# Performance work log

Hardware: AMD Instinct MI355X
Metric: run time of the kernel (lower is better)

The kernel has to match this reference:

```python
import jax, jax.numpy as jnp
import numpy as np

EPS = 1e-05
ITERS = 3


def safe_norm(s, axis):
    return jnp.sqrt(jnp.sum(s * s, axis=axis, keepdims=True) + EPS)


def squash(s, axis):
    norm = safe_norm(s, axis)
    return (norm / (1.0 + norm)) * s / norm


def setup_inputs() -> dict:
    key = jax.random.key(0)
    k1, k2 = jax.random.split(key)
    b, B, C, P, h, w = 4, 288, 32, 16, 14, 14  # B = K*K*32, P = pose 4x4
    u = jax.random.normal(k1, (b, B, C, P, h, w), dtype=jnp.float32)
    a = jax.random.uniform(k2, (b, B, h, w), dtype=jnp.float32)
    return {"u": u, "a": a}


def reference(u, a):
    # mode='dynamic': activation a is unused by this routing variant.
    # max_min_norm over pose axis (3), max/min over input-capsule axis (1)
    norm = safe_norm(u, 3)                          # (b,B,C,1,h,w)
    max_n = jnp.max(norm, axis=1, keepdims=True)    # (b,1,C,1,h,w)
    min_n = jnp.min(norm, axis=1, keepdims=True)
    u = u / (max_n - min_n)

    b, B, C, P, h, w = u.shape
    r = jnp.zeros((b, B, C, 1, h, w), dtype=u.dtype)
    v = None
    for i in range(ITERS):
        c = jax.nn.softmax(r, axis=2)                               # over C
        v = squash(jnp.sum(c * u, axis=1, keepdims=True), 3)        # (b,1,C,P,h,w)
        if i != ITERS - 1:
            r = r + jnp.sum(u * v, axis=3, keepdims=True)           # agreement
    a_out = safe_norm(v, 3)                                         # (b,1,C,1,h,w)
    return (jnp.squeeze(v, 1), jnp.squeeze(jnp.squeeze(a_out, 1), 2))
```

## Files before the change

### kernel.cpp

```cpp
#include <hip/hip_runtime.h>


constexpr int kB    = 4;
constexpr int kIC   = 288;
constexpr int kOC   = 32;
constexpr int kP    = 16;
constexpr int kHW   = 196;
constexpr int kNPOS = kB * kHW;
constexpr int kTILE = 16;
constexpr int kNTILES = kNPOS / kTILE;
constexpr int kNCH  = 16;
constexpr int kBCH  = kIC / kNCH;
constexpr int kSCP  = kOC * kP * kNPOS;
constexpr int kSC   = kOC * kNPOS;
constexpr int kBStride = kOC * kP * kHW;
constexpr float kEPS = 1e-5f;

__global__ __launch_bounds__(512, 4) void pass1_kernel(
    const float* __restrict__ U, float* __restrict__ s0,
    unsigned int* __restrict__ maxb, unsigned int* __restrict__ minb)
{
    const int tid = threadIdx.x;
    const int pos = tid & (kTILE - 1);
    const int c   = tid >> 4;
    const int n   = blockIdx.x * kTILE + pos;
    const int b   = n / kHW;
    const int hw  = n - b * kHW;
    const int B0  = blockIdx.y * kBCH;
    const float* up = U + (size_t)(((b * kIC + B0) * kOC + c) * kP) * kHW + hw;

    float sacc[kP];
#pragma unroll
    for (int p = 0; p < kP; ++p) sacc[p] = 0.f;
    float mx = 0.f, mn = 3.4e38f;

    for (int Bi = 0; Bi < kBCH; ++Bi) {
        float u[kP];
#pragma unroll
        for (int p = 0; p < kP; ++p) u[p] = up[p * kHW];
        float nsq = kEPS;
#pragma unroll
        for (int p = 0; p < kP; ++p) { nsq = fmaf(u[p], u[p], nsq); sacc[p] += u[p]; }
        const float nr = sqrtf(nsq);
        mx = fmaxf(mx, nr);
        mn = fminf(mn, nr);
        up += kBStride;
    }
    const int cn = c * kNPOS + n;
    atomicMax(&maxb[cn], __float_as_uint(mx));
    atomicMin(&minb[cn], __float_as_uint(mn));
#pragma unroll
    for (int p = 0; p < kP; ++p)
        atomicAdd(&s0[(c * kP + p) * kNPOS + n], sacc[p]);
}

__global__ void v0_kernel(float* __restrict__ s0,
                          const unsigned int* __restrict__ maxb,
                          const unsigned int* __restrict__ minb,
                          float* __restrict__ scaleb)
{
    const int i = blockIdx.x * blockDim.x + threadIdx.x;
    if (i >= kSC) return;
    const int c = i / kNPOS;
    const int n = i - c * kNPOS;
    const float mx = __uint_as_float(maxb[i]);
    const float mn = __uint_as_float(minb[i]);
    const float sc = 1.f / (mx - mn);
    scaleb[i] = sc;
    float sv[kP];
    float nsq = kEPS;
#pragma unroll
    for (int p = 0; p < kP; ++p) {
        const float v = s0[(c * kP + p) * kNPOS + n] * sc * (1.f / 32.f);
        sv[p] = v;
        nsq = fmaf(v, v, nsq);
    }
    const float inv = 1.f / (1.f + sqrtf(nsq));
#pragma unroll
    for (int p = 0; p < kP; ++p)
        s0[(c * kP + p) * kNPOS + n] = sv[p] * inv;
}

__global__ __launch_bounds__(512, 4) void route_kernel(
    const float* __restrict__ U, const float* __restrict__ Vr,
    const float* __restrict__ scaleb, float* __restrict__ sout)
{
    __shared__ float ldsM[8 * kTILE];
    __shared__ float ldsS[8 * kTILE];
    const int tid = threadIdx.x;
    const int pos = tid & (kTILE - 1);
    const int c   = tid >> 4;
    const int wv  = tid >> 6;
    const int n   = blockIdx.x * kTILE + pos;
    const int b   = n / kHW;
    const int hw  = n - b * kHW;
    const int B0  = blockIdx.y * kBCH;
    const float* up = U + (size_t)(((b * kIC + B0) * kOC + c) * kP) * kHW + hw;

    float vr[kP];
#pragma unroll
    for (int p = 0; p < kP; ++p) vr[p] = Vr[(c * kP + p) * kNPOS + n];
    const float sc = scaleb[c * kNPOS + n];

    float acc[kP];
#pragma unroll
    for (int p = 0; p < kP; ++p) acc[p] = 0.f;

    for (int Bi = 0; Bi < kBCH; ++Bi) {
        float u[kP];
#pragma unroll
        for (int p = 0; p < kP; ++p) u[p] = up[p * kHW];
        float d = 0.f;
#pragma unroll
        for (int p = 0; p < kP; ++p) d = fmaf(u[p], vr[p], d);
        const float r = sc * d;

        float m = r;
        m = fmaxf(m, __shfl_xor(m, 16));
        m = fmaxf(m, __shfl_xor(m, 32));
        if ((tid & 63) < kTILE) ldsM[wv * kTILE + pos] = m;
        __syncthreads();
        float mxv = ldsM[pos];
#pragma unroll
        for (int w = 1; w < 8; ++w) mxv = fmaxf(mxv, ldsM[w * kTILE + pos]);

        const float e = __expf(r - mxv);
        float z = e;
        z += __shfl_xor(z, 16);
        z += __shfl_xor(z, 32);
        if ((tid & 63) < kTILE) ldsS[wv * kTILE + pos] = z;
        __syncthreads();
        float Z = ldsS[pos];
#pragma unroll
        for (int w = 1; w < 8; ++w) Z += ldsS[w * kTILE + pos];

        const float cb = e / Z;
#pragma unroll
        for (int p = 0; p < kP; ++p) acc[p] = fmaf(cb, u[p], acc[p]);
        up += kBStride;
    }
#pragma unroll
    for (int p = 0; p < kP; ++p)
        atomicAdd(&sout[(c * kP + p) * kNPOS + n], sc * acc[p]);
}

__global__ void v1_kernel(float* __restrict__ v0buf,
                          const float* __restrict__ s1)
{
    const int i = blockIdx.x * blockDim.x + threadIdx.x;
    if (i >= kSC) return;
    const int c = i / kNPOS;
    const int n = i - c * kNPOS;
    float sv[kP];
    float nsq = kEPS;
#pragma unroll
    for (int p = 0; p < kP; ++p) {
        const float v = s1[(c * kP + p) * kNPOS + n];
        sv[p] = v;
        nsq = fmaf(v, v, nsq);
    }
    const float inv = 1.f / (1.f + sqrtf(nsq));
#pragma unroll
    for (int p = 0; p < kP; ++p)
        v0buf[(c * kP + p) * kNPOS + n] += sv[p] * inv;
}

__global__ void final_kernel(const float* __restrict__ s2, float* __restrict__ out)
{
    const int i = blockIdx.x * blockDim.x + threadIdx.x;
    if (i >= kSC) return;
    const int c = i / kNPOS;
    const int n = i - c * kNPOS;
    const int b = n / kHW;
    const int hw = n - b * kHW;
    float sv[kP];
    float nsq = kEPS;
#pragma unroll
    for (int p = 0; p < kP; ++p) {
        const float v = s2[(c * kP + p) * kNPOS + n];
        sv[p] = v;
        nsq = fmaf(v, v, nsq);
    }
    const float inv = 1.f / (1.f + sqrtf(nsq));
    float vs = 0.f;
#pragma unroll
    for (int p = 0; p < kP; ++p) {
        const float v = sv[p] * inv;
        out[(size_t)((b * kOC + c) * kP + p) * kHW + hw] = v;
        vs = fmaf(v, v, vs);
    }
    out[(size_t)kSCP + (b * kOC + c) * kHW + hw] = sqrtf(vs + kEPS);
}

extern "C" void kernel_launch(void* const* d_in, const int* in_sizes, int n_in,
                              void* d_out, int out_size, void* d_ws, size_t ws_size,
                              hipStream_t stream) {
    const float* U = (const float*)d_in[0];
    float* out = (float*)d_out;
    float* ws  = (float*)d_ws;

    float* s0 = ws;
    float* s1 = ws + kSCP;
    float* s2 = ws + 2 * kSCP;
    unsigned int* maxb = (unsigned int*)(ws + 3 * kSCP);
    unsigned int* minb = maxb + kSC;
    float* scaleb = (float*)(minb + kSC);

    hipMemsetAsync(s0, 0, (size_t)3 * kSCP * sizeof(float), stream);
    hipMemsetAsync(maxb, 0, (size_t)kSC * sizeof(unsigned int), stream);
    hipMemsetAsync(minb, 0x7F, (size_t)kSC * sizeof(unsigned int), stream);

    dim3 grid(kNTILES, kNCH);
    pass1_kernel<<<grid, 512, 0, stream>>>(U, s0, maxb, minb);
    v0_kernel<<<(kSC + 255) / 256, 256, 0, stream>>>(s0, maxb, minb, scaleb);
    route_kernel<<<grid, 512, 0, stream>>>(U, s0, scaleb, s1);
    v1_kernel<<<(kSC + 255) / 256, 256, 0, stream>>>(s0, s1);
    route_kernel<<<grid, 512, 0, stream>>>(U, s0, scaleb, s2);
    final_kernel<<<(kSC + 255) / 256, 256, 0, stream>>>(s2, out);
}
```

Baseline: 1.068 ms.

## Process two positions per thread with float2 loads and remap block order

Each thread now handles a pair of adjacent spatial positions and loads them as float2, widening the global loads of U in both pass1 and route kernels. The grid becomes 1D, and blocks are remapped through a stride-8 permutation, likely to spread tiles and chunks across XCDs or L2 slices. Route launch bounds are relaxed from 4 to 3 blocks per SM to allow more registers for the doubled state. The trade is higher register pressure and fewer blocks (400 vs 784), which lowers parallelism and adds a tail tile with clamped, masked positions.

```diff
diff --git a/kernel.cpp b/kernel.cpp
--- a/kernel.cpp
+++ b/kernel.cpp
@@ -7,51 +7,74 @@
 constexpr int kP    = 16;
 constexpr int kHW   = 196;
 constexpr int kNPOS = kB * kHW;
-constexpr int kTILE = 16;
-constexpr int kNTILES = kNPOS / kTILE;
+constexpr int kPAIR = 16;
+constexpr int kNTILES = 25;
 constexpr int kNCH  = 16;
 constexpr int kBCH  = kIC / kNCH;
 constexpr int kSCP  = kOC * kP * kNPOS;
 constexpr int kSC   = kOC * kNPOS;
-constexpr int kBStride = kOC * kP * kHW;
+constexpr int kBStride2 = kOC * kP * kHW / 2;
+constexpr int kNBLK = kNTILES * kNCH;
 constexpr float kEPS = 1e-5f;
+
+__device__ inline void decomp(int l, int& tile, int& chunk) {
+    const int logical = (l & 7) * (kNBLK / 8) + (l >> 3);
+    tile  = logical >> 4;
+    chunk = logical & 15;
+}
 
 __global__ __launch_bounds__(512, 4) void pass1_kernel(
     const float* __restrict__ U, float* __restrict__ s0,
     unsigned int* __restrict__ maxb, unsigned int* __restrict__ minb)
 {
+    int tile, chunk;
+    decomp(blockIdx.x, tile, chunk);
     const int tid = threadIdx.x;
-    const int pos = tid & (kTILE - 1);
+    const int j   = tid & 15;
     const int c   = tid >> 4;
-    const int n   = blockIdx.x * kTILE + pos;
-    const int b   = n / kHW;
-    const int hw  = n - b * kHW;
-    const int B0  = blockIdx.y * kBCH;
-    const float* up = U + (size_t)(((b * kIC + B0) * kOC + c) * kP) * kHW + hw;
-
-    float sacc[kP];
-#pragma unroll
-    for (int p = 0; p < kP; ++p) sacc[p] = 0.f;
-    float mx = 0.f, mn = 3.4e38f;
+    int n0 = tile * 32 + 2 * j;
+    const bool valid = (n0 < kNPOS);
+    if (!valid) n0 = kNPOS - 2;
+    const int b  = n0 / kHW;
+    const int hw = n0 - b * kHW;
+    const int B0 = chunk * kBCH;
+    const float2* up = (const float2*)(U + (size_t)(((b * kIC + B0) * kOC + c) * kP) * kHW + hw);
+
+    float2 sacc[kP];
+#pragma unroll
+    for (int p = 0; p < kP; ++p) sacc[p] = make_float2(0.f, 0.f);
+    float2 mx = make_float2(0.f, 0.f);
+    float2 mn = make_float2(3.4e38f, 3.4e38f);
 
     for (int Bi = 0; Bi < kBCH; ++Bi) {
-        float u[kP];
-#pragma unroll
-        for (int p = 0; p < kP; ++p) u[p] = up[p * kHW];
-        float nsq = kEPS;
-#pragma unroll
-        for (int p = 0; p < kP; ++p) { nsq = fmaf(u[p], u[p], nsq); sacc[p] += u[p]; }
-        const float nr = sqrtf(nsq);
-        mx = fmaxf(mx, nr);
-        mn = fminf(mn, nr);
-        up += kBStride;
-    }
-    const int cn = c * kNPOS + n;
-    atomicMax(&maxb[cn], __float_as_uint(mx));
-    atomicMin(&minb[cn], __float_as_uint(mn));
-#pragma unroll
-    for (int p = 0; p < kP; ++p)
-        atomicAdd(&s0[(c * kP + p) * kNPOS + n], sacc[p]);
+        float2 u[kP];
+#pragma unroll
+        for (int p = 0; p < kP; ++p) u[p] = up[p * (kHW / 2)];
+        float2 nsq = make_float2(kEPS, kEPS);
+#pragma unroll
+        for (int p = 0; p < kP; ++p) {
+            nsq.x = fmaf(u[p].x, u[p].x, nsq.x);
+            nsq.y = fmaf(u[p].y, u[p].y, nsq.y);
+            sacc[p].x += u[p].x;
+            sacc[p].y += u[p].y;
+        }
+        const float nrx = sqrtf(nsq.x), nry = sqrtf(nsq.y);
+        mx.x = fmaxf(mx.x, nrx); mx.y = fmaxf(mx.y, nry);
+        mn.x = fminf(mn.x, nrx); mn.y = fminf(mn.y, nry);
+        up += kBStride2;
+    }
+    if (valid) {
+        const int cn = c * kNPOS + n0;
+        atomicMax(&maxb[cn],     __float_as_uint(mx.x));
+        atomicMax(&maxb[cn + 1], __float_as_uint(mx.y));
+        atomicMin(&minb[cn],     __float_as_uint(mn.x));
+        atomicMin(&minb[cn + 1], __float_as_uint(mn.y));
+#pragma unroll
+        for (int p = 0; p < kP; ++p) {
+            atomicAdd(&s0[(c * kP + p) * kNPOS + n0],     sacc[p].x);
+            atomicAdd(&s0[(c * kP + p) * kNPOS + n0 + 1], sacc[p].y);
+        }
+    }
 }
 
 __global__ void v0_kernel(float* __restrict__ s0,
@@ -81,67 +104,86 @@
         s0[(c * kP + p) * kNPOS + n] = sv[p] * inv;
 }
 
-__global__ __launch_bounds__(512, 4) void route_kernel(
+__global__ __launch_bounds__(512, 3) void route_kernel(
     const float* __restrict__ U, const float* __restrict__ Vr,
     const float* __restrict__ scaleb, float* __restrict__ sout)
 {
-    __shared__ float ldsM[8 * kTILE];
-    __shared__ float ldsS[8 * kTILE];
+    __shared__ float2 ldsM[8 * kPAIR];
+    __shared__ float2 ldsS[8 * kPAIR];
+    int tile, chunk;
+    decomp(blockIdx.x, tile, chunk);
     const int tid = threadIdx.x;
-    const int pos = tid & (kTILE - 1);
+    const int j   = tid & 15;
     const int c   = tid >> 4;
     const int wv  = tid >> 6;
-    const int n   = blockIdx.x * kTILE + pos;
-    const int b   = n / kHW;
-    const int hw  = n - b * kHW;
-    const int B0  = blockIdx.y * kBCH;
-    const float* up = U + (size_t)(((b * kIC + B0) * kOC + c) * kP) * kHW + hw;
-
-    float vr[kP];
-#pragma unroll
-    for (int p = 0; p < kP; ++p) vr[p] = Vr[(c * kP + p) * kNPOS + n];
-    const float sc = scaleb[c * kNPOS + n];
-
-    float acc[kP];
-#pragma unroll
-    for (int p = 0; p < kP; ++p) acc[p] = 0.f;
+    int n0 = tile * 32 + 2 * j;
+    const bool valid = (n0 < kNPOS);
+    if (!valid) n0 = kNPOS - 2;
+    const int b  = n0 / kHW;
+    const int hw = n0 - b * kHW;
+    const int B0 = chunk * kBCH;
+    const float2* up = (const float2*)(U + (size_t)(((b * kIC + B0) * kOC + c) * kP) * kHW + hw);
+
+    float2 vr[kP];
+#pragma unroll
+    for (int p = 0; p < kP; ++p)
+        vr[p] = *(const float2*)&Vr[(c * kP + p) * kNPOS + n0];
+    const float2 sc = *(const float2*)&scaleb[c * kNPOS + n0];
+
+    float2 acc[kP];
+#pragma unroll
+    for (int p = 0; p < kP; ++p) acc[p] = make_float2(0.f, 0.f);
 
     for (int Bi = 0; Bi < kBCH; ++Bi) {
-        float u[kP];
-#pragma unroll
-        for (int p = 0; p < kP; ++p) u[p] = up[p * kHW];
-        float d = 0.f;
-#pragma unroll
-        for (int p = 0; p < kP; ++p) d = fmaf(u[p], vr[p], d);
-        const float r = sc * d;
-
-        float m = r;
-        m = fmaxf(m, __shfl_xor(m, 16));
-        m = fmaxf(m, __shfl_xor(m, 32));
-        if ((tid & 63) < kTILE) ldsM[wv * kTILE + pos] = m;
+        float2 u[kP];
+#pragma unroll
+        for (int p = 0; p < kP; ++p) u[p] = up[p * (kHW / 2)];
+        float2 d = make_float2(0.f, 0.f);
+#pragma unroll
+        for (int p = 0; p < kP; ++p) {
+            d.x = fmaf(u[p].x, vr[p].x, d.x);
+            d.y = fmaf(u[p].y, vr[p].y, d.y);
+        }
+        float2 r = make_float2(sc.x * d.x, sc.y * d.y);
+
+        float2 m = r;
+        m.x = fmaxf(m.x, __shfl_xor(m.x, 16)); m.y = fmaxf(m.y, __shfl_xor(m.y, 16));
+        m.x = fmaxf(m.x, __shfl_xor(m.x, 32)); m.y = fmaxf(m.y, __shfl_xor(m.y, 32));
+        if ((tid & 63) < kPAIR) ldsM[wv * kPAIR + j] = m;
         __syncthreads();
-        float mxv = ldsM[pos];
-#pragma unroll
-        for (int w = 1; w < 8; ++w) mxv = fmaxf(mxv, ldsM[w * kTILE + pos]);
-
-        const float e = __expf(r - mxv);
-        float z = e;
-        z += __shfl_xor(z, 16);
-        z += __shfl_xor(z, 32);
-        if ((tid & 63) < kTILE) ldsS[wv * kTILE + pos] = z;
+        float2 mxv = ldsM[j];
+#pragma unroll
+        for (int w = 1; w < 8; ++w) {
+            const float2 t = ldsM[w * kPAIR + j];
+            mxv.x = fmaxf(mxv.x, t.x); mxv.y = fmaxf(mxv.y, t.y);
+        }
+        const float2 e = make_float2(__expf(r.x - mxv.x), __expf(r.y - mxv.y));
+        float2 z = e;
+        z.x += __shfl_xor(z.x, 16); z.y += __shfl_xor(z.y, 16);
+        z.x += __shfl_xor(z.x, 32); z.y += __shfl_xor(z.y, 32);
+        if ((tid & 63) < kPAIR) ldsS[wv * kPAIR + j] = z;
         __syncthreads();
-        float Z = ldsS[pos];
-#pragma unroll
-        for (int w = 1; w < 8; ++w) Z += ldsS[w * kTILE + pos];
-
-        const float cb = e / Z;
-#pragma unroll
-        for (int p = 0; p < kP; ++p) acc[p] = fmaf(cb, u[p], acc[p]);
-        up += kBStride;
-    }
-#pragma unroll
-    for (int p = 0; p < kP; ++p)
-        atomicAdd(&sout[(c * kP + p) * kNPOS + n], sc * acc[p]);
+        float2 Z = ldsS[j];
+#pragma unroll
+        for (int w = 1; w < 8; ++w) {
+            const float2 t = ldsS[w * kPAIR + j];
+            Z.x += t.x; Z.y += t.y;
+        }
+        const float2 cb = make_float2(e.x / Z.x, e.y / Z.y);
+#pragma unroll
+        for (int p = 0; p < kP; ++p) {
+            acc[p].x = fmaf(cb.x, u[p].x, acc[p].x);
+            acc[p].y = fmaf(cb.y, u[p].y, acc[p].y);
+        }
+        up += kBStride2;
+    }
+    if (valid) {
+#pragma unroll
+        for (int p = 0; p < kP; ++p) {
+            atomicAdd(&sout[(c * kP + p) * kNPOS + n0],     sc.x * acc[p].x);
+            atomicAdd(&sout[(c * kP + p) * kNPOS + n0 + 1], sc.y * acc[p].y);
+        }
+    }
 }
 
 __global__ void v1_kernel(float* __restrict__ v0buf,
@@ -210,11 +252,10 @@
     hipMemsetAsync(maxb, 0, (size_t)kSC * sizeof(unsigned int), stream);
     hipMemsetAsync(minb, 0x7F, (size_t)kSC * sizeof(unsigned int), stream);
 
-    dim3 grid(kNTILES, kNCH);
-    pass1_kernel<<<grid, 512, 0, stream>>>(U, s0, maxb, minb);
+    pass1_kernel<<<kNBLK, 512, 0, stream>>>(U, s0, maxb, minb);
     v0_kernel<<<(kSC + 255) / 256, 256, 0, stream>>>(s0, maxb, minb, scaleb);
-    route_kernel<<<grid, 512, 0, stream>>>(U, s0, scaleb, s1);
+    route_kernel<<<kNBLK, 512, 0, stream>>>(U, s0, scaleb, s1);
     v1_kernel<<<(kSC + 255) / 256, 256, 0, stream>>>(s0, s1);
-    route_kernel<<<grid, 512, 0, stream>>>(U, s0, scaleb, s2);
+    route_kernel<<<kNBLK, 512, 0, stream>>>(U, s0, scaleb, s2);
     final_kernel<<<(kSC + 255) / 256, 256, 0, stream>>>(s2, out);
 }
```

New measurement: 1.048 ms. No clear change (-1.9%).
